# Kernel optimization log

Hardware: AMD Instinct MI355X
Metric: run time of the kernel (lower is better)

The kernel has to match this reference:

```python
import jax, jax.numpy as jnp
import numpy as np

L, D, H, K, M = 4, 512, 8, 10, 2048  # depth, dim, heads, relation bins, mlp_dim
DH = D // H
B, N = 4, 512
EPS = 1e-5


def setup_inputs() -> dict:
    key = jax.random.key(0)
    ks = jax.random.split(key, 12)
    s = lambda i, shape, scale: jax.random.normal(ks[i], shape, jnp.float32) * scale
    return {
        "x": s(0, (B, N, D), 1.0),
        "coord": jax.random.uniform(ks[1], (B, N, 2), dtype=jnp.float32) * 20.0,  # spread over ~K distance bins
        "ln1_g": jnp.ones((L, D)), "ln1_b": jnp.zeros((L, D)),
        "wq": s(2, (L, D, D), 0.02), "bq": jnp.zeros((L, D)),
        "wk": s(3, (L, D, D), 0.02), "bk": jnp.zeros((L, D)),
        "wv": s(4, (L, D, D), 0.02), "bv": jnp.zeros((L, D)),
        "wo": s(5, (L, D, D), 0.02), "bo": jnp.zeros((L, D)),
        "rel_k": s(6, (L, K, DH), 0.02), "rel_v": s(7, (L, K, DH), 0.02),
        "ln2_g": jnp.ones((L, D)), "ln2_b": jnp.zeros((L, D)),
        "w1": s(8, (L, D, M), 0.02), "b1": jnp.zeros((L, M)),
        "w2": s(9, (L, M, D), 0.02), "b2": jnp.zeros((L, D)),
        "lnf_g": jnp.ones((D,)), "lnf_b": jnp.zeros((D,)),
    }


def _ln(x, g, b):
    m = jnp.mean(x, -1, keepdims=True)
    v = jnp.mean((x - m) ** 2, -1, keepdims=True)
    return (x - m) * jax.lax.rsqrt(v + EPS) * g + b


def _forward(x, coord, ln1_g, ln1_b, wq, bq, wk, bk, wv, bv, wo, bo,
             rel_k, rel_v, ln2_g, ln2_b, w1, b1, w2, b2, lnf_g, lnf_b):
    b_, n_, _ = x.shape
    # pairwise Euclidean distances bucketized + clipped to K relation bins
    dist = jnp.linalg.norm(coord[:, :, None, :] - coord[:, None, :, :], axis=-1)  # [B,N,N]
    idx = jnp.clip(jnp.floor(dist), 0, K - 1).astype(jnp.int32)                   # [B,N,N]
    scale = DH ** -0.5
    for l in range(L):
        h = _ln(x, ln1_g[l], ln1_b[l])
        q = (h @ wq[l] + bq[l]).reshape(b_, n_, H, DH).transpose(0, 2, 1, 3)  # [B,H,N,DH]
        k = (h @ wk[l] + bk[l]).reshape(b_, n_, H, DH).transpose(0, 2, 1, 3)
        v = (h @ wv[l] + bv[l]).reshape(b_, n_, H, DH).transpose(0, 2, 1, 3)
        aK = rel_k[l][idx]  # [B,N,N,DH] relation key embeddings
        aV = rel_v[l][idx]  # [B,N,N,DH] relation value embeddings
        scores = (jnp.einsum('bhnd,bhmd->bhnm', q, k)
                  + jnp.einsum('bhnd,bnmd->bhnm', q, aK)) * scale
        attn = jax.nn.softmax(scores, axis=-1)  # [B,H,N,N]
        o = (jnp.einsum('bhnm,bhmd->bhnd', attn, v)
             + jnp.einsum('bhnm,bnmd->bhnd', attn, aV))
        o = o.transpose(0, 2, 1, 3).reshape(b_, n_, D) @ wo[l] + bo[l]
        x = o + x  # residual around attention
        h2 = _ln(x, ln2_g[l], ln2_b[l])
        x = jax.nn.gelu(h2 @ w1[l] + b1[l], approximate=False) @ w2[l] + b2[l] + x  # FFN residual
    return _ln(x, lnf_g, lnf_b)


def reference(x, coord, ln1_g, ln1_b, wq, bq, wk, bk, wv, bv, wo, bo,
              rel_k, rel_v, ln2_g, ln2_b, w1, b1, w2, b2, lnf_g, lnf_b):
    return _forward(x, coord, ln1_g, ln1_b, wq, bq, wk, bk, wv, bv, wo, bo,
                    rel_k, rel_v, ln2_g, ln2_b, w1, b1, w2, b2, lnf_g, lnf_b)
```

## Files before the change

### kernel.cpp

```cpp
#include <hip/hip_runtime.h>
#include <cmath>

constexpr int Bx = 4, Nx = 512, Dx = 512, Hx = 8, DHx = 64, Kx = 10, Mx = 2048, Lx = 4;
constexpr float EPSx = 1e-5f;
typedef unsigned short u16;
typedef __attribute__((ext_vector_type(8))) short short8;
typedef __attribute__((ext_vector_type(4))) float f32x4;

__device__ __forceinline__ u16 f2bf(float f) {
  unsigned u = __builtin_bit_cast(unsigned, f);
  return (u16)((u + 0x7fffu + ((u >> 16) & 1u)) >> 16);
}
__device__ __forceinline__ float bf2f(u16 h) {
  unsigned u = ((unsigned)h) << 16;
  return __builtin_bit_cast(float, u);
}
__device__ __forceinline__ void gload16(const void* g, void* l) {
  __builtin_amdgcn_global_load_lds((const __attribute__((address_space(1))) void*)g,
                                   (__attribute__((address_space(3))) void*)l, 16, 0, 0);
}
__device__ __forceinline__ float wave_max(float v) {
  #pragma unroll
  for (int off = 1; off < 64; off <<= 1) v = fmaxf(v, __shfl_xor(v, off));
  return v;
}
__device__ __forceinline__ float wave_sum(float v) {
  #pragma unroll
  for (int off = 1; off < 64; off <<= 1) v += __shfl_xor(v, off);
  return v;
}

__global__ __launch_bounds__(256) void idx_kernel(const float* __restrict__ coord,
                                                  unsigned char* __restrict__ idx8) {
  int t = blockIdx.x * 256 + threadIdx.x;
  int m = t % Nx;
  int n = (t / Nx) % Nx;
  int b = t / (Nx * Nx);
  float dx = coord[(b * Nx + n) * 2 + 0] - coord[(b * Nx + m) * 2 + 0];
  float dy = coord[(b * Nx + n) * 2 + 1] - coord[(b * Nx + m) * 2 + 1];
  float dist = sqrtf(dx * dx + dy * dy);
  int bin = (int)floorf(dist);
  bin = bin < 0 ? 0 : (bin > Kx - 1 ? Kx - 1 : bin);
  idx8[t] = (unsigned char)bin;
}

__global__ __launch_bounds__(256) void wsplitT_kernel(const float* __restrict__ W,
                                                      u16* __restrict__ Thi,
                                                      u16* __restrict__ Tlo,
                                                      int K, int N, size_t dst_lstride) {
  __shared__ float tile[32][33];
  int l = blockIdx.z;
  const float* Wl = W + (size_t)l * K * N;
  u16* hi = Thi + (size_t)l * dst_lstride;
  u16* lo = Tlo + (size_t)l * dst_lstride;
  int n0 = blockIdx.x * 32, k0 = blockIdx.y * 32;
  int tx = threadIdx.x & 31, ty = threadIdx.x >> 5;
  #pragma unroll
  for (int i = 0; i < 4; i++) {
    int kk = ty + i * 8;
    tile[kk][tx] = Wl[(size_t)(k0 + kk) * N + n0 + tx];
  }
  __syncthreads();
  #pragma unroll
  for (int i = 0; i < 4; i++) {
    int nn = ty + i * 8;
    float v = tile[tx][nn];
    u16 h = f2bf(v);
    hi[(size_t)(n0 + nn) * K + k0 + tx] = h;
    lo[(size_t)(n0 + nn) * K + k0 + tx] = f2bf(v - bf2f(h));
  }
}

__global__ __launch_bounds__(256) void ln_kernel(const float* __restrict__ x,
                                                 const float* __restrict__ g,
                                                 const float* __restrict__ bta,
                                                 float* __restrict__ out) {
  __shared__ float red[256];
  int row = blockIdx.x;
  int tid = threadIdx.x;
  const float2 v = reinterpret_cast<const float2*>(x + (size_t)row * Dx)[tid];

  red[tid] = v.x + v.y;
  __syncthreads();
  for (int s = 128; s > 0; s >>= 1) { if (tid < s) red[tid] += red[tid + s]; __syncthreads(); }
  float mean = red[0] * (1.0f / Dx);
  __syncthreads();

  float d0 = v.x - mean, d1 = v.y - mean;
  red[tid] = d0 * d0 + d1 * d1;
  __syncthreads();
  for (int s = 128; s > 0; s >>= 1) { if (tid < s) red[tid] += red[tid + s]; __syncthreads(); }
  float rstd = rsqrtf(red[0] * (1.0f / Dx) + EPSx);
  __syncthreads();

  float2 gg = reinterpret_cast<const float2*>(g)[tid];
  float2 bb = reinterpret_cast<const float2*>(bta)[tid];
  float2 o;
  o.x = d0 * rstd * gg.x + bb.x;
  o.y = d1 * rstd * gg.y + bb.y;
  reinterpret_cast<float2*>(out + (size_t)row * Dx)[tid] = o;
}

__global__ __launch_bounds__(256) void ln_split_kernel(const float* __restrict__ x,
                                                       const float* __restrict__ g,
                                                       const float* __restrict__ bta,
                                                       u16* __restrict__ hhi,
                                                       u16* __restrict__ hlo) {
  __shared__ float red[256];
  int row = blockIdx.x;
  int tid = threadIdx.x;
  const float2 v = reinterpret_cast<const float2*>(x + (size_t)row * Dx)[tid];

  red[tid] = v.x + v.y;
  __syncthreads();
  for (int s = 128; s > 0; s >>= 1) { if (tid < s) red[tid] += red[tid + s]; __syncthreads(); }
  float mean = red[0] * (1.0f / Dx);
  __syncthreads();

  float d0 = v.x - mean, d1 = v.y - mean;
  red[tid] = d0 * d0 + d1 * d1;
  __syncthreads();
  for (int s = 128; s > 0; s >>= 1) { if (tid < s) red[tid] += red[tid + s]; __syncthreads(); }
  float rstd = rsqrtf(red[0] * (1.0f / Dx) + EPSx);
  __syncthreads();

  float2 gg = reinterpret_cast<const float2*>(g)[tid];
  float2 bb = reinterpret_cast<const float2*>(bta)[tid];
  float ox = d0 * rstd * gg.x + bb.x;
  float oy = d1 * rstd * gg.y + bb.y;
  u16 hx = f2bf(ox), hy = f2bf(oy);
  ushort2 hv = {hx, hy};
  ushort2 lv = {f2bf(ox - bf2f(hx)), f2bf(oy - bf2f(hy))};
  reinterpret_cast<ushort2*>(hhi + (size_t)row * Dx)[tid] = hv;
  reinterpret_cast<ushort2*>(hlo + (size_t)row * Dx)[tid] = lv;
}

template <int BM, int BN, int EPI>
__global__ __launch_bounds__(256) void gemm_mfma(
    const u16* __restrict__ Ahi, const u16* __restrict__ Alo,
    const u16* __restrict__ Bhi, const u16* __restrict__ Blo,
    const float* __restrict__ bias,
    float* __restrict__ C, u16* __restrict__ Chi, u16* __restrict__ Clo,
    int M, int Nn, int Kk) {
  constexpr int FM = BM / 32, FN = BN / 32;
  __shared__ __align__(16) u16 lds[(BM + BN) * 64];
  u16* lAhi = lds;
  u16* lAlo = lds + BM * 32;
  u16* lBhi = lds + BM * 64;
  u16* lBlo = lds + BM * 64 + BN * 32;

  const int tid = threadIdx.x;
  const int lane = tid & 63;
  const int wid = tid >> 6;
  const int wr = wid >> 1, wc = wid & 1;
  const int row0 = blockIdx.y * BM, col0 = blockIdx.x * BN;
  const int kg = (lane >> 4) * 8;
  const int lr = lane & 15;

  f32x4 acc[FM][FN];
  #pragma unroll
  for (int m = 0; m < FM; m++)
    #pragma unroll
    for (int n = 0; n < FN; n++) acc[m][n] = (f32x4)(0.0f);

  constexpr int AR = (BM * 32) / 2048;
  constexpr int BR = (BN * 32) / 2048;

  for (int kt = 0; kt < Kk; kt += 32) {
    #pragma unroll
    for (int r = 0; r < AR; r++) {
      int e = r * 2048 + tid * 8;
      int row = e >> 5, kc = e & 31;
      size_t go = (size_t)(row0 + row) * Kk + kt + kc;
      gload16(Ahi + go, lAhi + e);
      gload16(Alo + go, lAlo + e);
    }
    #pragma unroll
    for (int r = 0; r < BR; r++) {
      int e = r * 2048 + tid * 8;
      int row = e >> 5, kc = e & 31;
      size_t go = (size_t)(col0 + row) * Kk + kt + kc;
      gload16(Bhi + go, lBhi + e);
      gload16(Blo + go, lBlo + e);
    }
    __syncthreads();

    short8 ah[FM], al[FM], bh[FN], bl[FN];
    #pragma unroll
    for (int m = 0; m < FM; m++) {
      int off = (wr * (BM / 2) + m * 16 + lr) * 32 + kg;
      ah[m] = *reinterpret_cast<const short8*>(lAhi + off);
      al[m] = *reinterpret_cast<const short8*>(lAlo + off);
    }
    #pragma unroll
    for (int n = 0; n < FN; n++) {
      int off = (wc * (BN / 2) + n * 16 + lr) * 32 + kg;
      bh[n] = *reinterpret_cast<const short8*>(lBhi + off);
      bl[n] = *reinterpret_cast<const short8*>(lBlo + off);
    }
    #pragma unroll
    for (int m = 0; m < FM; m++)
      #pragma unroll
      for (int n = 0; n < FN; n++) {
        acc[m][n] = __builtin_amdgcn_mfma_f32_16x16x32_bf16(ah[m], bh[n], acc[m][n], 0, 0, 0);
        acc[m][n] = __builtin_amdgcn_mfma_f32_16x16x32_bf16(ah[m], bl[n], acc[m][n], 0, 0, 0);
        acc[m][n] = __builtin_amdgcn_mfma_f32_16x16x32_bf16(al[m], bh[n], acc[m][n], 0, 0, 0);
      }
    __syncthreads();
  }

  const int rbase = (lane >> 4) * 4;
  #pragma unroll
  for (int m = 0; m < FM; m++) {
    #pragma unroll
    for (int n = 0; n < FN; n++) {
      int cidx = col0 + wc * (BN / 2) + n * 16 + lr;
      float bcol = bias[cidx];
      #pragma unroll
      for (int r = 0; r < 4; r++) {
        int row = row0 + wr * (BM / 2) + m * 16 + rbase + r;
        size_t o = (size_t)row * Nn + cidx;
        float val = acc[m][n][r] + bcol;
        if constexpr (EPI == 1) {
          C[o] = val + C[o];
        } else if constexpr (EPI == 2) {
          val = 0.5f * val * (1.0f + erff(val * 0.70710678118654752f));
          u16 h = f2bf(val);
          Chi[o] = h;
          Clo[o] = f2bf(val - bf2f(h));
        } else {
          u16 h = f2bf(val);
          Chi[o] = h;
          Clo[o] = f2bf(val - bf2f(h));
        }
      }
    }
  }
}

template <int KC>
__global__ __launch_bounds__(256) void gemm_splitk(
    const u16* __restrict__ Ahi, const u16* __restrict__ Alo,
    const u16* __restrict__ Bhi, const u16* __restrict__ Blo,
    const float* __restrict__ bias, float* __restrict__ C,
    int M, int Nn, int Kk) {
  constexpr int BM = 64, BN = 128;
  constexpr int FM = 2, FN = 4;
  __shared__ __align__(16) u16 lds[(BM + BN) * 64];
  u16* lAhi = lds;
  u16* lAlo = lds + BM * 32;
  u16* lBhi = lds + BM * 64;
  u16* lBlo = lds + BM * 64 + BN * 32;

  const int tid = threadIdx.x;
  const int lane = tid & 63;
  const int wid = tid >> 6;
  const int wr = wid >> 1, wc = wid & 1;
  const int row0 = blockIdx.y * BM, col0 = blockIdx.x * BN;
  const int kz = blockIdx.z;
  const int kbase = kz * KC;
  const int kg = (lane >> 4) * 8;
  const int lr = lane & 15;

  f32x4 acc[FM][FN];
  #pragma unroll
  for (int m = 0; m < FM; m++)
    #pragma unroll
    for (int n = 0; n < FN; n++) acc[m][n] = (f32x4)(0.0f);

  for (int kt = kbase; kt < kbase + KC; kt += 32) {
    {
      int e = tid * 8;
      int row = e >> 5, kc = e & 31;
      size_t go = (size_t)(row0 + row) * Kk + kt + kc;
      gload16(Ahi + go, lAhi + e);
      gload16(Alo + go, lAlo + e);
    }
    #pragma unroll
    for (int r = 0; r < 2; r++) {
      int e = r * 2048 + tid * 8;
      int row = e >> 5, kc = e & 31;
      size_t go = (size_t)(col0 + row) * Kk + kt + kc;
      gload16(Bhi + go, lBhi + e);
      gload16(Blo + go, lBlo + e);
    }
    __syncthreads();

    short8 ah[FM], al[FM], bh[FN], bl[FN];
    #pragma unroll
    for (int m = 0; m < FM; m++) {
      int off = (wr * 32 + m * 16 + lr) * 32 + kg;
      ah[m] = *reinterpret_cast<const short8*>(lAhi + off);
      al[m] = *reinterpret_cast<const short8*>(lAlo + off);
    }
    #pragma unroll
    for (int n = 0; n < FN; n++) {
      int off = (wc * 64 + n * 16 + lr) * 32 + kg;
      bh[n] = *reinterpret_cast<const short8*>(lBhi + off);
      bl[n] = *reinterpret_cast<const short8*>(lBlo + off);
    }
    #pragma unroll
    for (int m = 0; m < FM; m++)
      #pragma unroll
      for (int n = 0; n < FN; n++) {
        acc[m][n] = __builtin_amdgcn_mfma_f32_16x16x32_bf16(ah[m], bh[n], acc[m][n], 0, 0, 0);
        acc[m][n] = __builtin_amdgcn_mfma_f32_16x16x32_bf16(ah[m], bl[n], acc[m][n], 0, 0, 0);
        acc[m][n] = __builtin_amdgcn_mfma_f32_16x16x32_bf16(al[m], bh[n], acc[m][n], 0, 0, 0);
      }
    __syncthreads();
  }

  const int rbase = (lane >> 4) * 4;
  #pragma unroll
  for (int m = 0; m < FM; m++) {
    #pragma unroll
    for (int n = 0; n < FN; n++) {
      int cidx = col0 + wc * 64 + n * 16 + lr;
      float bcol = (kz == 0) ? bias[cidx] : 0.0f;
      #pragma unroll
      for (int r = 0; r < 4; r++) {
        int row = row0 + wr * 32 + m * 16 + rbase + r;
        atomicAdd(&C[(size_t)row * Nn + cidx], acc[m][n][r] + bcol);
      }
    }
  }
}

__global__ __launch_bounds__(256) void gemm_qkv(
    const u16* __restrict__ Ahi, const u16* __restrict__ Alo,
    const u16* __restrict__ Bhi, const u16* __restrict__ Blo,
    const float* __restrict__ bq, const float* __restrict__ bk,
    const float* __restrict__ bv,
    u16* __restrict__ qhi, u16* __restrict__ qlo,
    u16* __restrict__ khi, u16* __restrict__ klo,
    u16* __restrict__ vThi, u16* __restrict__ vTlo) {
  constexpr int Kk = 512;
  __shared__ __align__(16) u16 lds[128 * 64];
  u16* lAhi = lds;
  u16* lAlo = lds + 2048;
  u16* lBhi = lds + 4096;
  u16* lBlo = lds + 6144;

  const int tid = threadIdx.x;
  const int lane = tid & 63;
  const int wid = tid >> 6;
  const int wr = wid >> 1, wc = wid & 1;
  const int row0 = blockIdx.y * 64, col0 = blockIdx.x * 64;
  const int kg = (lane >> 4) * 8;
  const int lr = lane & 15;

  f32x4 acc[2][2];
  #pragma unroll
  for (int m = 0; m < 2; m++)
    #pragma unroll
    for (int n = 0; n < 2; n++) acc[m][n] = (f32x4)(0.0f);

  for (int kt = 0; kt < Kk; kt += 32) {
    int e = tid * 8;
    int row = e >> 5, kc = e & 31;
    size_t ga = (size_t)(row0 + row) * Kk + kt + kc;
    size_t gb = (size_t)(col0 + row) * Kk + kt + kc;
    gload16(Ahi + ga, lAhi + e);
    gload16(Alo + ga, lAlo + e);
    gload16(Bhi + gb, lBhi + e);
    gload16(Blo + gb, lBlo + e);
    __syncthreads();

    short8 ah[2], al[2], bh[2], bl[2];
    #pragma unroll
    for (int m = 0; m < 2; m++) {
      int off = (wr * 32 + m * 16 + lr) * 32 + kg;
      ah[m] = *reinterpret_cast<const short8*>(lAhi + off);
      al[m] = *reinterpret_cast<const short8*>(lAlo + off);
    }
    #pragma unroll
    for (int n = 0; n < 2; n++) {
      int off = (wc * 32 + n * 16 + lr) * 32 + kg;
      bh[n] = *reinterpret_cast<const short8*>(lBhi + off);
      bl[n] = *reinterpret_cast<const short8*>(lBlo + off);
    }
    #pragma unroll
    for (int m = 0; m < 2; m++)
      #pragma unroll
      for (int n = 0; n < 2; n++) {
        acc[m][n] = __builtin_amdgcn_mfma_f32_16x16x32_bf16(ah[m], bh[n], acc[m][n], 0, 0, 0);
        acc[m][n] = __builtin_amdgcn_mfma_f32_16x16x32_bf16(ah[m], bl[n], acc[m][n], 0, 0, 0);
        acc[m][n] = __builtin_amdgcn_mfma_f32_16x16x32_bf16(al[m], bh[n], acc[m][n], 0, 0, 0);
      }
    __syncthreads();
  }

  const int rbase = (lane >> 4) * 4;
  #pragma unroll
  for (int m = 0; m < 2; m++) {
    #pragma unroll
    for (int n = 0; n < 2; n++) {
      int cidx = col0 + wc * 32 + n * 16 + lr;
      float bcol = cidx < 512 ? bq[cidx]
                  : (cidx < 1024 ? bk[cidx - 512] : bv[cidx - 1024]);
      #pragma unroll
      for (int r = 0; r < 4; r++) {
        int row = row0 + wr * 32 + m * 16 + rbase + r;
        float val = acc[m][n][r] + bcol;
        u16 h = f2bf(val);
        u16 lo2 = f2bf(val - bf2f(h));
        if (cidx < 512) {
          size_t o = (size_t)row * 512 + cidx;
          qhi[o] = h; qlo[o] = lo2;
        } else if (cidx < 1024) {
          size_t o = (size_t)row * 512 + (cidx - 512);
          khi[o] = h; klo[o] = lo2;
        } else {
          size_t o = (size_t)(cidx - 1024) * 2048 + row;
          vThi[o] = h; vTlo[o] = lo2;
        }
      }
    }
  }
}

__global__ __launch_bounds__(256) void qrel_kernel(const u16* __restrict__ qhi,
                                                   const u16* __restrict__ qlo,
                                                   const float* __restrict__ relk,
                                                   float* __restrict__ qrel) {
  int t = blockIdx.x * 256 + threadIdx.x;
  if (t >= Bx * Nx * Hx * Kx) return;
  int kbin = t % Kx;
  int h = (t / Kx) % Hx;
  int bn = t / (Kx * Hx);
  size_t base = (size_t)bn * Dx + h * DHx;
  const float* rr = relk + kbin * DHx;
  float s = 0.f;
  #pragma unroll
  for (int d = 0; d < DHx; d++)
    s += (bf2f(qhi[base + d]) + bf2f(qlo[base + d])) * rr[d];
  qrel[t] = s;
}

__global__ __launch_bounds__(256) void scores_mfma(
    const u16* __restrict__ qhi, const u16* __restrict__ qlo,
    const u16* __restrict__ khi, const u16* __restrict__ klo,
    const float* __restrict__ qrel, const unsigned char* __restrict__ idx8,
    float* __restrict__ scores) {
  __shared__ __align__(16) u16 lds[4 * 2048];
  u16* lQh = lds;
  u16* lQl = lds + 2048;
  u16* lKh = lds + 4096;
  u16* lKl = lds + 6144;

  const int bh = blockIdx.z;
  const int b = bh >> 3, h = bh & 7;
  const int n0 = blockIdx.y * 64, m0 = blockIdx.x * 64;
  const int tid = threadIdx.x;
  const int lane = tid & 63;
  const int wid = tid >> 6;
  const int wr = wid >> 1, wc = wid & 1;
  const int kg = (lane >> 4) * 8;
  const int lr = lane & 15;

  f32x4 acc[2][2];
  #pragma unroll
  for (int m = 0; m < 2; m++)
    #pragma unroll
    for (int n = 0; n < 2; n++) acc[m][n] = (f32x4)(0.0f);

  for (int kt = 0; kt < DHx; kt += 32) {
    int e = tid * 8;
    int row = e >> 5, kc = e & 31;
    size_t gq = (size_t)(b * Nx + n0 + row) * Dx + h * DHx + kt + kc;
    size_t gk = (size_t)(b * Nx + m0 + row) * Dx + h * DHx + kt + kc;
    gload16(qhi + gq, lQh + e);
    gload16(qlo + gq, lQl + e);
    gload16(khi + gk, lKh + e);
    gload16(klo + gk, lKl + e);
    __syncthreads();

    short8 ah[2], al[2], bhf[2], blf[2];
    #pragma unroll
    for (int m = 0; m < 2; m++) {
      int off = (wr * 32 + m * 16 + lr) * 32 + kg;
      ah[m] = *reinterpret_cast<const short8*>(lQh + off);
      al[m] = *reinterpret_cast<const short8*>(lQl + off);
    }
    #pragma unroll
    for (int n = 0; n < 2; n++) {
      int off = (wc * 32 + n * 16 + lr) * 32 + kg;
      bhf[n] = *reinterpret_cast<const short8*>(lKh + off);
      blf[n] = *reinterpret_cast<const short8*>(lKl + off);
    }
    #pragma unroll
    for (int m = 0; m < 2; m++)
      #pragma unroll
      for (int n = 0; n < 2; n++) {
        acc[m][n] = __builtin_amdgcn_mfma_f32_16x16x32_bf16(ah[m], bhf[n], acc[m][n], 0, 0, 0);
        acc[m][n] = __builtin_amdgcn_mfma_f32_16x16x32_bf16(ah[m], blf[n], acc[m][n], 0, 0, 0);
        acc[m][n] = __builtin_amdgcn_mfma_f32_16x16x32_bf16(al[m], bhf[n], acc[m][n], 0, 0, 0);
      }
    __syncthreads();
  }

  const int rbase = (lane >> 4) * 4;
  #pragma unroll
  for (int m = 0; m < 2; m++) {
    #pragma unroll
    for (int n = 0; n < 2; n++) {
      int mg = m0 + wc * 32 + n * 16 + lr;
      #pragma unroll
      for (int r = 0; r < 4; r++) {
        int ng = n0 + wr * 32 + m * 16 + rbase + r;
        unsigned char iv = idx8[(size_t)(b * Nx + ng) * Nx + mg];
        float bias = qrel[((size_t)(b * Nx + ng) * Hx + h) * Kx + iv];
        scores[((size_t)bh * Nx + ng) * Nx + mg] = (acc[m][n][r] + bias) * 0.125f;
      }
    }
  }
}

__global__ __launch_bounds__(256) void softmax_wave(float* scores,
                                                    const unsigned char* __restrict__ idx8,
                                                    float* __restrict__ attnK) {
  const int tid = threadIdx.x;
  const int lane = tid & 63;
  const int wid = tid >> 6;
  const int row = blockIdx.x * 4 + wid;
  const int n = row & (Nx - 1);
  const int b = row >> 12;
  float* s = scores + (size_t)row * Nx;

  float4 v0 = reinterpret_cast<const float4*>(s)[lane * 2];
  float4 v1 = reinterpret_cast<const float4*>(s)[lane * 2 + 1];
  float p[8] = {v0.x, v0.y, v0.z, v0.w, v1.x, v1.y, v1.z, v1.w};

  float mx = p[0];
  #pragma unroll
  for (int j = 1; j < 8; j++) mx = fmaxf(mx, p[j]);
  mx = wave_max(mx);

  float sum = 0.f;
  #pragma unroll
  for (int j = 0; j < 8; j++) { p[j] = expf(p[j] - mx); sum += p[j]; }
  sum = wave_sum(sum);
  float inv = 1.0f / sum;

  const unsigned char* idr = idx8 + (size_t)(b * Nx + n) * Nx + lane * 8;
  uchar4 c0 = *reinterpret_cast<const uchar4*>(idr);
  uchar4 c1 = *reinterpret_cast<const uchar4*>(idr + 4);
  int iv[8] = {c0.x, c0.y, c0.z, c0.w, c1.x, c1.y, c1.z, c1.w};

  float bins[Kx];
  #pragma unroll
  for (int kk = 0; kk < Kx; kk++) bins[kk] = 0.f;
  #pragma unroll
  for (int j = 0; j < 8; j++)
    #pragma unroll
    for (int kk = 0; kk < Kx; kk++) bins[kk] += (iv[j] == kk) ? p[j] : 0.f;
  #pragma unroll
  for (int kk = 0; kk < Kx; kk++) bins[kk] = wave_sum(bins[kk]);

  short8 sv;
  #pragma unroll
  for (int j = 0; j < 8; j++) sv[j] = (short)f2bf(p[j] * inv);
  u16* prow = reinterpret_cast<u16*>(s);
  *reinterpret_cast<short8*>(prow + lane * 8) = sv;

  if (lane == 0) {
    #pragma unroll
    for (int kk = 0; kk < Kx; kk++) attnK[(size_t)row * Kx + kk] = bins[kk] * inv;
  }
}

__global__ __launch_bounds__(256) void pv_mfma(
    const u16* __restrict__ P,
    const u16* __restrict__ vThi, const u16* __restrict__ vTlo,
    const float* __restrict__ attnK, const float* __restrict__ rel_v,
    u16* __restrict__ ohi, u16* __restrict__ olo) {
  __shared__ __align__(16) u16 lP[2048], lVh[2048], lVl[2048];
  __shared__ float aKs[64][Kx];
  __shared__ float RelVs[Kx][DHx];

  const int bh = blockIdx.y;
  const int b = bh >> 3, h = bh & 7;
  const int n0 = blockIdx.x * 64;
  const int tid = threadIdx.x;
  const int lane = tid & 63;
  const int wid = tid >> 6;
  const int wr = wid >> 1, wc = wid & 1;
  const int kg = (lane >> 4) * 8;
  const int lr = lane & 15;

  for (int t = tid; t < 64 * Kx; t += 256)
    aKs[t / Kx][t % Kx] = attnK[(size_t)(bh * Nx + n0 + t / Kx) * Kx + t % Kx];
  for (int t = tid; t < Kx * DHx; t += 256)
    RelVs[t / DHx][t % DHx] = rel_v[t];

  f32x4 acc[2][2];
  #pragma unroll
  for (int m = 0; m < 2; m++)
    #pragma unroll
    for (int n = 0; n < 2; n++) acc[m][n] = (f32x4)(0.0f);

  for (int mt = 0; mt < Nx; mt += 32) {
    int e = tid * 8;
    int row = e >> 5, kc = e & 31;
    gload16(P + (size_t)(bh * Nx + n0 + row) * 1024 + mt + kc, lP + e);
    size_t gv = (size_t)(h * DHx + row) * 2048 + b * Nx + mt + kc;
    gload16(vThi + gv, lVh + e);
    gload16(vTlo + gv, lVl + e);
    __syncthreads();

    short8 pa[2], bvh[2], bvl[2];
    #pragma unroll
    for (int m = 0; m < 2; m++) {
      int off = (wr * 32 + m * 16 + lr) * 32 + kg;
      pa[m] = *reinterpret_cast<const short8*>(lP + off);
    }
    #pragma unroll
    for (int n = 0; n < 2; n++) {
      int off = (wc * 32 + n * 16 + lr) * 32 + kg;
      bvh[n] = *reinterpret_cast<const short8*>(lVh + off);
      bvl[n] = *reinterpret_cast<const short8*>(lVl + off);
    }
    #pragma unroll
    for (int m = 0; m < 2; m++)
      #pragma unroll
      for (int n = 0; n < 2; n++) {
        acc[m][n] = __builtin_amdgcn_mfma_f32_16x16x32_bf16(pa[m], bvh[n], acc[m][n], 0, 0, 0);
        acc[m][n] = __builtin_amdgcn_mfma_f32_16x16x32_bf16(pa[m], bvl[n], acc[m][n], 0, 0, 0);
      }
    __syncthreads();
  }

  const int rbase = (lane >> 4) * 4;
  #pragma unroll
  for (int n = 0; n < 2; n++) {
    int dl = wc * 32 + n * 16 + lr;
    float rv[Kx];
    #pragma unroll
    for (int kk = 0; kk < Kx; kk++) rv[kk] = RelVs[kk][dl];
    #pragma unroll
    for (int m = 0; m < 2; m++) {
      #pragma unroll
      for (int r = 0; r < 4; r++) {
        int nl = wr * 32 + m * 16 + rbase + r;
        float val = acc[m][n][r];
        #pragma unroll
        for (int kk = 0; kk < Kx; kk++) val += aKs[nl][kk] * rv[kk];
        size_t oo = (size_t)(b * Nx + n0 + nl) * Dx + h * DHx + dl;
        u16 hh = f2bf(val);
        ohi[oo] = hh;
        olo[oo] = f2bf(val - bf2f(hh));
      }
    }
  }
}

extern "C" void kernel_launch(void* const* d_in, const int* in_sizes, int n_in,
                              void* d_out, int out_size, void* d_ws, size_t ws_size,
                              hipStream_t stream) {
  const float* x_in  = (const float*)d_in[0];
  const float* coord = (const float*)d_in[1];
  const float* ln1_g = (const float*)d_in[2];
  const float* ln1_b = (const float*)d_in[3];
  const float* wq    = (const float*)d_in[4];
  const float* bq    = (const float*)d_in[5];
  const float* wk    = (const float*)d_in[6];
  const float* bk    = (const float*)d_in[7];
  const float* wv    = (const float*)d_in[8];
  const float* bv    = (const float*)d_in[9];
  const float* wo    = (const float*)d_in[10];
  const float* bo    = (const float*)d_in[11];
  const float* rel_k = (const float*)d_in[12];
  const float* rel_v = (const float*)d_in[13];
  const float* ln2_g = (const float*)d_in[14];
  const float* ln2_b = (const float*)d_in[15];
  const float* w1    = (const float*)d_in[16];
  const float* b1    = (const float*)d_in[17];
  const float* w2    = (const float*)d_in[18];
  const float* b2    = (const float*)d_in[19];
  const float* lnf_g = (const float*)d_in[20];
  const float* lnf_b = (const float*)d_in[21];

  float* x = (float*)d_out;
  constexpr size_t BND  = (size_t)Bx * Nx * Dx;
  constexpr size_t SC   = (size_t)Bx * Hx * Nx * Nx;
  constexpr size_t RELS = (size_t)Bx * Nx * Hx * Kx;
  constexpr size_t QKVW = (size_t)1536 * 512;

  char* w = (char*)d_ws;
  size_t off = 0;
  auto nxt = [&](size_t bytes) -> void* {
    void* p = w + off;
    off = (off + bytes + 255) & ~(size_t)255;
    return p;
  };
  unsigned char* idxb = (unsigned char*)nxt((size_t)Bx * Nx * Nx);
  float* scores = (float*)nxt(4ull * SC);
  float* qrel   = (float*)nxt(4ull * RELS);
  float* attnK  = (float*)nxt(4ull * RELS);
  u16* qhi = (u16*)nxt(2ull * BND);
  u16* qlo = (u16*)nxt(2ull * BND);
  u16* khi = (u16*)nxt(2ull * BND);
  u16* klo = (u16*)nxt(2ull * BND);
  u16* vThi = (u16*)nxt(2ull * BND);
  u16* vTlo = (u16*)nxt(2ull * BND);
  u16* hhi = (u16*)nxt(2ull * BND);
  u16* hlo = (u16*)nxt(2ull * BND);
  u16* ohi = (u16*)nxt(2ull * BND);
  u16* olo = (u16*)nxt(2ull * BND);
  u16* wqkvThi = (u16*)nxt(2ull * Lx * QKVW);
  u16* wqkvTlo = (u16*)nxt(2ull * Lx * QKVW);
  u16* woThi = (u16*)nxt(2ull * Lx * Dx * Dx);
  u16* woTlo = (u16*)nxt(2ull * Lx * Dx * Dx);
  u16* w1Thi = (u16*)nxt(2ull * Lx * Dx * Mx);
  u16* w1Tlo = (u16*)nxt(2ull * Lx * Dx * Mx);
  u16* w2Thi = (u16*)nxt(2ull * Lx * Mx * Dx);
  u16* w2Tlo = (u16*)nxt(2ull * Lx * Mx * Dx);
  u16* f1hi = (u16*)scores;
  u16* f1lo = f1hi + (size_t)(Bx * Nx) * Mx;
  u16* Pbuf = (u16*)scores;

  hipMemcpyAsync(x, x_in, BND * sizeof(float), hipMemcpyDeviceToDevice, stream);
  idx_kernel<<<(Bx * Nx * Nx) / 256, 256, 0, stream>>>(coord, idxb);

  dim3 gw(Dx / 32, Dx / 32, Lx);
  wsplitT_kernel<<<gw, 256, 0, stream>>>(wq, wqkvThi, wqkvTlo, Dx, Dx, QKVW);
  wsplitT_kernel<<<gw, 256, 0, stream>>>(wk, wqkvThi + (size_t)512 * 512,
                                         wqkvTlo + (size_t)512 * 512, Dx, Dx, QKVW);
  wsplitT_kernel<<<gw, 256, 0, stream>>>(wv, wqkvThi + (size_t)1024 * 512,
                                         wqkvTlo + (size_t)1024 * 512, Dx, Dx, QKVW);
  wsplitT_kernel<<<gw, 256, 0, stream>>>(wo, woThi, woTlo, Dx, Dx, (size_t)Dx * Dx);
  wsplitT_kernel<<<dim3(Mx / 32, Dx / 32, Lx), 256, 0, stream>>>(
      w1, w1Thi, w1Tlo, Dx, Mx, (size_t)Dx * Mx);
  wsplitT_kernel<<<dim3(Dx / 32, Mx / 32, Lx), 256, 0, stream>>>(
      w2, w2Thi, w2Tlo, Mx, Dx, (size_t)Mx * Dx);

  const int Mrows = Bx * Nx;
  dim3 gqkv(1536 / 64, Mrows / 64);
  dim3 gw1(Mx / 128, Mrows / 64);
  dim3 gwo(Dx / 128, Mrows / 64, 4);
  dim3 gw2(Dx / 128, Mrows / 64, 4);
  dim3 gs(Nx / 64, Nx / 64, Bx * Hx);
  dim3 gpv(Nx / 64, Bx * Hx);

  for (int l = 0; l < Lx; l++) {
    size_t wD = (size_t)l * Dx * Dx;
    size_t w1o = (size_t)l * Dx * Mx;
    size_t w2o = (size_t)l * Mx * Dx;

    ln_split_kernel<<<Mrows, 256, 0, stream>>>(x, ln1_g + l * Dx, ln1_b + l * Dx, hhi, hlo);
    gemm_qkv<<<gqkv, 256, 0, stream>>>(hhi, hlo,
                                       wqkvThi + (size_t)l * QKVW, wqkvTlo + (size_t)l * QKVW,
                                       bq + l * Dx, bk + l * Dx, bv + l * Dx,
                                       qhi, qlo, khi, klo, vThi, vTlo);
    qrel_kernel<<<(Bx * Nx * Hx * Kx + 255) / 256, 256, 0, stream>>>(
        qhi, qlo, rel_k + (size_t)l * Kx * DHx, qrel);
    scores_mfma<<<gs, 256, 0, stream>>>(qhi, qlo, khi, klo, qrel, idxb, scores);
    softmax_wave<<<Bx * Hx * Nx / 4, 256, 0, stream>>>(scores, idxb, attnK);
    pv_mfma<<<gpv, 256, 0, stream>>>(Pbuf, vThi, vTlo, attnK,
                                     rel_v + (size_t)l * Kx * DHx, ohi, olo);
    gemm_splitk<128><<<gwo, 256, 0, stream>>>(ohi, olo, woThi + wD, woTlo + wD,
                                              bo + l * Dx, x, Mrows, Dx, Dx);
    ln_split_kernel<<<Mrows, 256, 0, stream>>>(x, ln2_g + l * Dx, ln2_b + l * Dx, hhi, hlo);
    gemm_mfma<64, 128, 2><<<gw1, 256, 0, stream>>>(hhi, hlo, w1Thi + w1o, w1Tlo + w1o,
                                                   b1 + l * Mx, nullptr, f1hi, f1lo,
                                                   Mrows, Mx, Dx);
    gemm_splitk<512><<<gw2, 256, 0, stream>>>(f1hi, f1lo, w2Thi + w2o, w2Tlo + w2o,
                                              b2 + l * Dx, x, Mrows, Dx, Mx);
  }
  ln_kernel<<<Mrows, 256, 0, stream>>>(x, lnf_g, lnf_b, x);
}
```

Measured before the change: 793.7 us.

## Fuse scores, softmax and PV into one attention kernel with LDS-resident rows

Replaces the separate scores, softmax, and PV kernels with a single kernel per 32-query tile per head. Full 512-wide score rows and bf16 probabilities stay in shared memory, so the fp32 score matrix and attnK buffer no longer round-trip through global memory and two launches go away. The cost is heavy LDS use (about 64KB for scores plus 33KB for P), which limits occupancy to roughly one block per CU. It also reduces the grid to 512 blocks and serializes the phases inside each block.

```diff
diff --git a/kernel.cpp b/kernel.cpp
--- a/kernel.cpp
+++ b/kernel.cpp
@@ -437,219 +437,180 @@
   qrel[t] = s;
 }
 
-__global__ __launch_bounds__(256) void scores_mfma(
+__global__ __launch_bounds__(256) void attn_fused(
     const u16* __restrict__ qhi, const u16* __restrict__ qlo,
     const u16* __restrict__ khi, const u16* __restrict__ klo,
+    const u16* __restrict__ vThi, const u16* __restrict__ vTlo,
     const float* __restrict__ qrel, const unsigned char* __restrict__ idx8,
-    float* __restrict__ scores) {
-  __shared__ __align__(16) u16 lds[4 * 2048];
-  u16* lQh = lds;
-  u16* lQl = lds + 2048;
-  u16* lKh = lds + 4096;
-  u16* lKl = lds + 6144;
-
-  const int bh = blockIdx.z;
+    const float* __restrict__ rel_v,
+    u16* __restrict__ ohi, u16* __restrict__ olo) {
+  __shared__ float sc[32][512];
+  __shared__ u16 lP[32][520];
+  __shared__ __align__(16) u16 stg[4][2048];
+  __shared__ float binsS[32][Kx];
+  __shared__ float RelVs[Kx][DHx];
+
+  const int bh = blockIdx.y;
   const int b = bh >> 3, h = bh & 7;
-  const int n0 = blockIdx.y * 64, m0 = blockIdx.x * 64;
+  const int n0 = blockIdx.x * 32;
   const int tid = threadIdx.x;
   const int lane = tid & 63;
   const int wid = tid >> 6;
   const int wr = wid >> 1, wc = wid & 1;
   const int kg = (lane >> 4) * 8;
   const int lr = lane & 15;
-
-  f32x4 acc[2][2];
-  #pragma unroll
-  for (int m = 0; m < 2; m++)
-    #pragma unroll
-    for (int n = 0; n < 2; n++) acc[m][n] = (f32x4)(0.0f);
-
-  for (int kt = 0; kt < DHx; kt += 32) {
-    int e = tid * 8;
-    int row = e >> 5, kc = e & 31;
-    size_t gq = (size_t)(b * Nx + n0 + row) * Dx + h * DHx + kt + kc;
-    size_t gk = (size_t)(b * Nx + m0 + row) * Dx + h * DHx + kt + kc;
-    gload16(qhi + gq, lQh + e);
-    gload16(qlo + gq, lQl + e);
-    gload16(khi + gk, lKh + e);
-    gload16(klo + gk, lKl + e);
-    __syncthreads();
-
-    short8 ah[2], al[2], bhf[2], blf[2];
-    #pragma unroll
-    for (int m = 0; m < 2; m++) {
-      int off = (wr * 32 + m * 16 + lr) * 32 + kg;
-      ah[m] = *reinterpret_cast<const short8*>(lQh + off);
-      al[m] = *reinterpret_cast<const short8*>(lQl + off);
-    }
-    #pragma unroll
-    for (int n = 0; n < 2; n++) {
-      int off = (wc * 32 + n * 16 + lr) * 32 + kg;
-      bhf[n] = *reinterpret_cast<const short8*>(lKh + off);
-      blf[n] = *reinterpret_cast<const short8*>(lKl + off);
-    }
-    #pragma unroll
-    for (int m = 0; m < 2; m++)
-      #pragma unroll
-      for (int n = 0; n < 2; n++) {
-        acc[m][n] = __builtin_amdgcn_mfma_f32_16x16x32_bf16(ah[m], bhf[n], acc[m][n], 0, 0, 0);
-        acc[m][n] = __builtin_amdgcn_mfma_f32_16x16x32_bf16(ah[m], blf[n], acc[m][n], 0, 0, 0);
-        acc[m][n] = __builtin_amdgcn_mfma_f32_16x16x32_bf16(al[m], bhf[n], acc[m][n], 0, 0, 0);
-      }
-    __syncthreads();
-  }
-
   const int rbase = (lane >> 4) * 4;
-  #pragma unroll
-  for (int m = 0; m < 2; m++) {
-    #pragma unroll
-    for (int n = 0; n < 2; n++) {
-      int mg = m0 + wc * 32 + n * 16 + lr;
+
+  for (int t = tid; t < Kx * DHx; t += 256)
+    RelVs[t / DHx][t % DHx] = rel_v[t];
+
+  short8 qh[2], ql[2];
+  {
+    size_t qb = (size_t)(b * Nx + n0 + wr * 16 + lr) * Dx + h * DHx + kg;
+    qh[0] = *reinterpret_cast<const short8*>(qhi + qb);
+    qh[1] = *reinterpret_cast<const short8*>(qhi + qb + 32);
+    ql[0] = *reinterpret_cast<const short8*>(qlo + qb);
+    ql[1] = *reinterpret_cast<const short8*>(qlo + qb + 32);
+  }
+
+  for (int mt = 0; mt < Nx; mt += 64) {
+    {
+      int e = tid * 8;
+      int row = e >> 5;
+      size_t kb = (size_t)(b * Nx + mt + row) * Dx + h * DHx + (e & 31);
+      gload16(khi + kb, &stg[0][e]);
+      gload16(khi + kb + 32, &stg[1][e]);
+      gload16(klo + kb, &stg[2][e]);
+      gload16(klo + kb + 32, &stg[3][e]);
+    }
+    __syncthreads();
+
+    f32x4 acc[2];
+    acc[0] = (f32x4)(0.0f);
+    acc[1] = (f32x4)(0.0f);
+    #pragma unroll
+    for (int f = 0; f < 2; f++) {
+      int boff = (wc * 32 + f * 16 + lr) * 32 + kg;
+      short8 kh0 = *reinterpret_cast<const short8*>(&stg[0][boff]);
+      short8 kh1 = *reinterpret_cast<const short8*>(&stg[1][boff]);
+      short8 kl0 = *reinterpret_cast<const short8*>(&stg[2][boff]);
+      short8 kl1 = *reinterpret_cast<const short8*>(&stg[3][boff]);
+      acc[f] = __builtin_amdgcn_mfma_f32_16x16x32_bf16(qh[0], kh0, acc[f], 0, 0, 0);
+      acc[f] = __builtin_amdgcn_mfma_f32_16x16x32_bf16(qh[1], kh1, acc[f], 0, 0, 0);
+      acc[f] = __builtin_amdgcn_mfma_f32_16x16x32_bf16(qh[0], kl0, acc[f], 0, 0, 0);
+      acc[f] = __builtin_amdgcn_mfma_f32_16x16x32_bf16(qh[1], kl1, acc[f], 0, 0, 0);
+      acc[f] = __builtin_amdgcn_mfma_f32_16x16x32_bf16(ql[0], kh0, acc[f], 0, 0, 0);
+      acc[f] = __builtin_amdgcn_mfma_f32_16x16x32_bf16(ql[1], kh1, acc[f], 0, 0, 0);
+    }
+    #pragma unroll
+    for (int f = 0; f < 2; f++) {
+      int mloc = wc * 32 + f * 16 + lr;
+      int mg = mt + mloc;
       #pragma unroll
       for (int r = 0; r < 4; r++) {
-        int ng = n0 + wr * 32 + m * 16 + rbase + r;
+        int nl = wr * 16 + rbase + r;
+        int ng = n0 + nl;
         unsigned char iv = idx8[(size_t)(b * Nx + ng) * Nx + mg];
         float bias = qrel[((size_t)(b * Nx + ng) * Hx + h) * Kx + iv];
-        scores[((size_t)bh * Nx + ng) * Nx + mg] = (acc[m][n][r] + bias) * 0.125f;
+        sc[nl][mg] = (acc[f][r] + bias) * 0.125f;
       }
     }
-  }
-}
-
-__global__ __launch_bounds__(256) void softmax_wave(float* scores,
-                                                    const unsigned char* __restrict__ idx8,
-                                                    float* __restrict__ attnK) {
-  const int tid = threadIdx.x;
-  const int lane = tid & 63;
-  const int wid = tid >> 6;
-  const int row = blockIdx.x * 4 + wid;
-  const int n = row & (Nx - 1);
-  const int b = row >> 12;
-  float* s = scores + (size_t)row * Nx;
-
-  float4 v0 = reinterpret_cast<const float4*>(s)[lane * 2];
-  float4 v1 = reinterpret_cast<const float4*>(s)[lane * 2 + 1];
-  float p[8] = {v0.x, v0.y, v0.z, v0.w, v1.x, v1.y, v1.z, v1.w};
-
-  float mx = p[0];
-  #pragma unroll
-  for (int j = 1; j < 8; j++) mx = fmaxf(mx, p[j]);
-  mx = wave_max(mx);
-
-  float sum = 0.f;
-  #pragma unroll
-  for (int j = 0; j < 8; j++) { p[j] = expf(p[j] - mx); sum += p[j]; }
-  sum = wave_sum(sum);
-  float inv = 1.0f / sum;
-
-  const unsigned char* idr = idx8 + (size_t)(b * Nx + n) * Nx + lane * 8;
-  uchar4 c0 = *reinterpret_cast<const uchar4*>(idr);
-  uchar4 c1 = *reinterpret_cast<const uchar4*>(idr + 4);
-  int iv[8] = {c0.x, c0.y, c0.z, c0.w, c1.x, c1.y, c1.z, c1.w};
-
-  float bins[Kx];
-  #pragma unroll
-  for (int kk = 0; kk < Kx; kk++) bins[kk] = 0.f;
-  #pragma unroll
-  for (int j = 0; j < 8; j++)
-    #pragma unroll
-    for (int kk = 0; kk < Kx; kk++) bins[kk] += (iv[j] == kk) ? p[j] : 0.f;
-  #pragma unroll
-  for (int kk = 0; kk < Kx; kk++) bins[kk] = wave_sum(bins[kk]);
-
-  short8 sv;
-  #pragma unroll
-  for (int j = 0; j < 8; j++) sv[j] = (short)f2bf(p[j] * inv);
-  u16* prow = reinterpret_cast<u16*>(s);
-  *reinterpret_cast<short8*>(prow + lane * 8) = sv;
-
-  if (lane == 0) {
-    #pragma unroll
-    for (int kk = 0; kk < Kx; kk++) attnK[(size_t)row * Kx + kk] = bins[kk] * inv;
-  }
-}
-
-__global__ __launch_bounds__(256) void pv_mfma(
-    const u16* __restrict__ P,
-    const u16* __restrict__ vThi, const u16* __restrict__ vTlo,
-    const float* __restrict__ attnK, const float* __restrict__ rel_v,
-    u16* __restrict__ ohi, u16* __restrict__ olo) {
-  __shared__ __align__(16) u16 lP[2048], lVh[2048], lVl[2048];
-  __shared__ float aKs[64][Kx];
-  __shared__ float RelVs[Kx][DHx];
-
-  const int bh = blockIdx.y;
-  const int b = bh >> 3, h = bh & 7;
-  const int n0 = blockIdx.x * 64;
-  const int tid = threadIdx.x;
-  const int lane = tid & 63;
-  const int wid = tid >> 6;
-  const int wr = wid >> 1, wc = wid & 1;
-  const int kg = (lane >> 4) * 8;
-  const int lr = lane & 15;
-
-  for (int t = tid; t < 64 * Kx; t += 256)
-    aKs[t / Kx][t % Kx] = attnK[(size_t)(bh * Nx + n0 + t / Kx) * Kx + t % Kx];
-  for (int t = tid; t < Kx * DHx; t += 256)
-    RelVs[t / DHx][t % DHx] = rel_v[t];
-
-  f32x4 acc[2][2];
-  #pragma unroll
-  for (int m = 0; m < 2; m++)
-    #pragma unroll
-    for (int n = 0; n < 2; n++) acc[m][n] = (f32x4)(0.0f);
-
-  for (int mt = 0; mt < Nx; mt += 32) {
-    int e = tid * 8;
-    int row = e >> 5, kc = e & 31;
-    gload16(P + (size_t)(bh * Nx + n0 + row) * 1024 + mt + kc, lP + e);
-    size_t gv = (size_t)(h * DHx + row) * 2048 + b * Nx + mt + kc;
-    gload16(vThi + gv, lVh + e);
-    gload16(vTlo + gv, lVl + e);
-    __syncthreads();
-
-    short8 pa[2], bvh[2], bvl[2];
-    #pragma unroll
-    for (int m = 0; m < 2; m++) {
-      int off = (wr * 32 + m * 16 + lr) * 32 + kg;
-      pa[m] = *reinterpret_cast<const short8*>(lP + off);
-    }
-    #pragma unroll
-    for (int n = 0; n < 2; n++) {
-      int off = (wc * 32 + n * 16 + lr) * 32 + kg;
-      bvh[n] = *reinterpret_cast<const short8*>(lVh + off);
-      bvl[n] = *reinterpret_cast<const short8*>(lVl + off);
-    }
-    #pragma unroll
-    for (int m = 0; m < 2; m++)
-      #pragma unroll
-      for (int n = 0; n < 2; n++) {
-        acc[m][n] = __builtin_amdgcn_mfma_f32_16x16x32_bf16(pa[m], bvh[n], acc[m][n], 0, 0, 0);
-        acc[m][n] = __builtin_amdgcn_mfma_f32_16x16x32_bf16(pa[m], bvl[n], acc[m][n], 0, 0, 0);
-      }
-    __syncthreads();
-  }
-
-  const int rbase = (lane >> 4) * 4;
-  #pragma unroll
-  for (int n = 0; n < 2; n++) {
-    int dl = wc * 32 + n * 16 + lr;
+    __syncthreads();
+  }
+
+  for (int rr = 0; rr < 8; rr++) {
+    int nl = wid * 8 + rr;
+    int ng = n0 + nl;
+    float4 v0 = *reinterpret_cast<const float4*>(&sc[nl][lane * 8]);
+    float4 v1 = *reinterpret_cast<const float4*>(&sc[nl][lane * 8 + 4]);
+    float p[8] = {v0.x, v0.y, v0.z, v0.w, v1.x, v1.y, v1.z, v1.w};
+
+    float mx = p[0];
+    #pragma unroll
+    for (int j = 1; j < 8; j++) mx = fmaxf(mx, p[j]);
+    mx = wave_max(mx);
+
+    float sum = 0.f;
+    #pragma unroll
+    for (int j = 0; j < 8; j++) { p[j] = expf(p[j] - mx); sum += p[j]; }
+    sum = wave_sum(sum);
+    float inv = 1.0f / sum;
+
+    const unsigned char* idr = idx8 + (size_t)(b * Nx + ng) * Nx + lane * 8;
+    uchar4 c0 = *reinterpret_cast<const uchar4*>(idr);
+    uchar4 c1 = *reinterpret_cast<const uchar4*>(idr + 4);
+    int iv[8] = {c0.x, c0.y, c0.z, c0.w, c1.x, c1.y, c1.z, c1.w};
+
+    float bins[Kx];
+    #pragma unroll
+    for (int kk = 0; kk < Kx; kk++) bins[kk] = 0.f;
+    #pragma unroll
+    for (int j = 0; j < 8; j++)
+      #pragma unroll
+      for (int kk = 0; kk < Kx; kk++) bins[kk] += (iv[j] == kk) ? p[j] : 0.f;
+    #pragma unroll
+    for (int kk = 0; kk < Kx; kk++) bins[kk] = wave_sum(bins[kk]);
+
+    short8 sv;
+    #pragma unroll
+    for (int j = 0; j < 8; j++) sv[j] = (short)f2bf(p[j] * inv);
+    *reinterpret_cast<short8*>(&lP[nl][lane * 8]) = sv;
+
+    if (lane == 0) {
+      #pragma unroll
+      for (int kk = 0; kk < Kx; kk++) binsS[nl][kk] = bins[kk] * inv;
+    }
+  }
+  __syncthreads();
+
+  f32x4 oacc[2];
+  oacc[0] = (f32x4)(0.0f);
+  oacc[1] = (f32x4)(0.0f);
+  for (int mt = 0; mt < Nx; mt += 64) {
+    {
+      int e = tid * 8;
+      int row = e >> 5;
+      size_t vb = (size_t)(h * DHx + row) * 2048 + b * Nx + mt + (e & 31);
+      gload16(vThi + vb, &stg[0][e]);
+      gload16(vThi + vb + 32, &stg[1][e]);
+      gload16(vTlo + vb, &stg[2][e]);
+      gload16(vTlo + vb + 32, &stg[3][e]);
+    }
+    __syncthreads();
+
+    short8 pa0 = *reinterpret_cast<const short8*>(&lP[wr * 16 + lr][mt + kg]);
+    short8 pa1 = *reinterpret_cast<const short8*>(&lP[wr * 16 + lr][mt + 32 + kg]);
+    #pragma unroll
+    for (int f = 0; f < 2; f++) {
+      int boff = (wc * 32 + f * 16 + lr) * 32 + kg;
+      short8 vh0 = *reinterpret_cast<const short8*>(&stg[0][boff]);
+      short8 vh1 = *reinterpret_cast<const short8*>(&stg[1][boff]);
+      short8 vl0 = *reinterpret_cast<const short8*>(&stg[2][boff]);
+      short8 vl1 = *reinterpret_cast<const short8*>(&stg[3][boff]);
+      oacc[f] = __builtin_amdgcn_mfma_f32_16x16x32_bf16(pa0, vh0, oacc[f], 0, 0, 0);
+      oacc[f] = __builtin_amdgcn_mfma_f32_16x16x32_bf16(pa1, vh1, oacc[f], 0, 0, 0);
+      oacc[f] = __builtin_amdgcn_mfma_f32_16x16x32_bf16(pa0, vl0, oacc[f], 0, 0, 0);
+      oacc[f] = __builtin_amdgcn_mfma_f32_16x16x32_bf16(pa1, vl1, oacc[f], 0, 0, 0);
+    }
+    __syncthreads();
+  }
+
+  #pragma unroll
+  for (int f = 0; f < 2; f++) {
+    int dl = wc * 32 + f * 16 + lr;
     float rv[Kx];
     #pragma unroll
     for (int kk = 0; kk < Kx; kk++) rv[kk] = RelVs[kk][dl];
     #pragma unroll
-    for (int m = 0; m < 2; m++) {
-      #pragma unroll
-      for (int r = 0; r < 4; r++) {
-        int nl = wr * 32 + m * 16 + rbase + r;
-        float val = acc[m][n][r];
-        #pragma unroll
-        for (int kk = 0; kk < Kx; kk++) val += aKs[nl][kk] * rv[kk];
-        size_t oo = (size_t)(b * Nx + n0 + nl) * Dx + h * DHx + dl;
-        u16 hh = f2bf(val);
-        ohi[oo] = hh;
-        olo[oo] = f2bf(val - bf2f(hh));
-      }
+    for (int r = 0; r < 4; r++) {
+      int nl = wr * 16 + rbase + r;
+      float val = oacc[f][r];
+      #pragma unroll
+      for (int kk = 0; kk < Kx; kk++) val += binsS[nl][kk] * rv[kk];
+      size_t oo = (size_t)(b * Nx + n0 + nl) * Dx + h * DHx + dl;
+      u16 hh = f2bf(val);
+      ohi[oo] = hh;
+      olo[oo] = f2bf(val - bf2f(hh));
     }
   }
 }
@@ -696,7 +657,6 @@
   unsigned char* idxb = (unsigned char*)nxt((size_t)Bx * Nx * Nx);
   float* scores = (float*)nxt(4ull * SC);
   float* qrel   = (float*)nxt(4ull * RELS);
-  float* attnK  = (float*)nxt(4ull * RELS);
   u16* qhi = (u16*)nxt(2ull * BND);
   u16* qlo = (u16*)nxt(2ull * BND);
   u16* khi = (u16*)nxt(2ull * BND);
@@ -717,7 +677,6 @@
   u16* w2Tlo = (u16*)nxt(2ull * Lx * Mx * Dx);
   u16* f1hi = (u16*)scores;
   u16* f1lo = f1hi + (size_t)(Bx * Nx) * Mx;
-  u16* Pbuf = (u16*)scores;
 
   hipMemcpyAsync(x, x_in, BND * sizeof(float), hipMemcpyDeviceToDevice, stream);
   idx_kernel<<<(Bx * Nx * Nx) / 256, 256, 0, stream>>>(coord, idxb);
@@ -739,8 +698,7 @@
   dim3 gw1(Mx / 128, Mrows / 64);
   dim3 gwo(Dx / 128, Mrows / 64, 4);
   dim3 gw2(Dx / 128, Mrows / 64, 4);
-  dim3 gs(Nx / 64, Nx / 64, Bx * Hx);
-  dim3 gpv(Nx / 64, Bx * Hx);
+  dim3 gat(Nx / 32, Bx * Hx);
 
   for (int l = 0; l < Lx; l++) {
     size_t wD = (size_t)l * Dx * Dx;
@@ -754,10 +712,9 @@
                                        qhi, qlo, khi, klo, vThi, vTlo);
     qrel_kernel<<<(Bx * Nx * Hx * Kx + 255) / 256, 256, 0, stream>>>(
         qhi, qlo, rel_k + (size_t)l * Kx * DHx, qrel);
-    scores_mfma<<<gs, 256, 0, stream>>>(qhi, qlo, khi, klo, qrel, idxb, scores);
-    softmax_wave<<<Bx * Hx * Nx / 4, 256, 0, stream>>>(scores, idxb, attnK);
-    pv_mfma<<<gpv, 256, 0, stream>>>(Pbuf, vThi, vTlo, attnK,
-                                     rel_v + (size_t)l * Kx * DHx, ohi, olo);
+    attn_fused<<<gat, 256, 0, stream>>>(qhi, qlo, khi, klo, vThi, vTlo,
+                                        qrel, idxb, rel_v + (size_t)l * Kx * DHx,
+                                        ohi, olo);
     gemm_splitk<128><<<gwo, 256, 0, stream>>>(ohi, olo, woThi + wD, woTlo + wD,
                                               bo + l * Dx, x, Mrows, Dx, Dx);
     ln_split_kernel<<<Mrows, 256, 0, stream>>>(x, ln2_g + l * Dx, ln2_b + l * Dx, hhi, hlo);
```

New measurement: 857.0 us. 8.0% more time.
